# Kernel optimization log

Hardware: AMD Instinct MI355X
Metric: run time of the kernel (lower is better)

Reference implementation:

```python
import jax, jax.numpy as jnp
import numpy as np

RESO = 192
BASIS_DIM = 9
DATA_DIM = BASIS_DIM * 3 + 1  # 28 = sigma + 9 SH coeffs x 3 color channels
N_PTS = 1_000_000
RADIUS = 1.0


def setup_inputs() -> dict:
    key = jax.random.key(0)
    k1, k2, k3 = jax.random.split(key, 3)
    capacity = RESO ** 3
    # world-space points in [-1.1, 1.1] to exercise the border clamping
    points = jax.random.uniform(k1, (N_PTS, 3), jnp.float32, -1.1, 1.1)
    data = jax.random.normal(k2, (capacity, DATA_DIM), jnp.float32) * 0.1
    links = jnp.arange(capacity, dtype=jnp.int32)
    keep = jax.random.uniform(k3, (capacity,)) < 0.7
    links = jnp.where(keep, links, jnp.int32(-1)).reshape(RESO, RESO, RESO)
    radius = jnp.full((3,), RADIUS, jnp.float32)
    center = jnp.zeros((3,), jnp.float32)
    offset = 0.5 * (1.0 - center / radius)   # SparseGrid._offset
    scaling = 0.5 / radius                   # SparseGrid._scaling
    return {"points": points, "data": data, "links": links,
            "offset": offset, "scaling": scaling}


def _trilerp(points, data, links, offset, scaling):
    # world2grid: p = points * (scaling*gsz) + (offset*gsz - 0.5)
    gsz = jnp.array(links.shape, dtype=points.dtype)  # [3]
    p = points * (scaling * gsz) + (offset * gsz - 0.5)
    # clamp_min 0, clamp_max gsz[i]-1 (border padding)
    p = jnp.clip(p, 0.0, gsz - 1.0)
    # integer cell (trunc == floor since p >= 0), clamped to gsz[i]-2
    l = jnp.minimum(p.astype(jnp.int32), jnp.array(links.shape, jnp.int32) - 2)
    wb = p - l.astype(p.dtype)  # [N,3] fractional weights
    wa = 1.0 - wb
    lx, ly, lz = l[:, 0], l[:, 1], l[:, 2]

    def fetch(ix, iy, iz):
        lk = links[ix, iy, iz]                       # [N] int32, -1 = empty
        vals = data[jnp.maximum(lk, 0)]              # [N, C] gather
        return jnp.where((lk >= 0)[:, None], vals, jnp.zeros_like(vals))

    c000 = fetch(lx, ly, lz)
    c001 = fetch(lx, ly, lz + 1)
    c010 = fetch(lx, ly + 1, lz)
    c011 = fetch(lx, ly + 1, lz + 1)
    c100 = fetch(lx + 1, ly, lz)
    c101 = fetch(lx + 1, ly, lz + 1)
    c110 = fetch(lx + 1, ly + 1, lz)
    c111 = fetch(lx + 1, ly + 1, lz + 1)

    wz_a, wz_b = wa[:, 2:3], wb[:, 2:3]
    c00 = c000 * wz_a + c001 * wz_b
    c01 = c010 * wz_a + c011 * wz_b
    c10 = c100 * wz_a + c101 * wz_b
    c11 = c110 * wz_a + c111 * wz_b
    wy_a, wy_b = wa[:, 1:2], wb[:, 1:2]
    c0 = c00 * wy_a + c01 * wy_b
    c1 = c10 * wy_a + c11 * wy_b
    return c0 * wa[:, 0:1] + c1 * wb[:, 0:1]  # [N, 28]


def reference(points, data, links, offset, scaling):
    return _trilerp(points, data, links, offset, scaling)
```

## Files before the change

### kernel.cpp

```cpp
#include <hip/hip_runtime.h>

#define RESO 192
#define DATA_DIM 28

typedef float f4 __attribute__((ext_vector_type(4)));

__global__ __launch_bounds__(256) void trilerp_kernel(
    const float* __restrict__ points,
    const float* __restrict__ data,
    const int*   __restrict__ links,
    const float* __restrict__ offset,
    const float* __restrict__ scaling,
    float*       __restrict__ out,
    int npts)
{
    const int gid   = blockIdx.x * blockDim.x + threadIdx.x;
    const int point = gid >> 3;
    const int sub   = threadIdx.x & 7;
    if (point >= npts) return;

    const float px = points[point * 3 + 0];
    const float py = points[point * 3 + 1];
    const float pz = points[point * 3 + 2];

    const float g = (float)RESO;

    float p0 = px * (scaling[0] * g) + (offset[0] * g - 0.5f);
    float p1 = py * (scaling[1] * g) + (offset[1] * g - 0.5f);
    float p2 = pz * (scaling[2] * g) + (offset[2] * g - 0.5f);

    p0 = fminf(fmaxf(p0, 0.0f), g - 1.0f);
    p1 = fminf(fmaxf(p1, 0.0f), g - 1.0f);
    p2 = fminf(fmaxf(p2, 0.0f), g - 1.0f);

    const int lx = min((int)p0, RESO - 2);
    const int ly = min((int)p1, RESO - 2);
    const int lz = min((int)p2, RESO - 2);

    const float wbx = p0 - (float)lx, wax = 1.0f - wbx;
    const float wby = p1 - (float)ly, way = 1.0f - wby;
    const float wbz = p2 - (float)lz, waz = 1.0f - wbz;

    const int base = (lx * RESO + ly) * RESO + lz;
    const int lk000 = links[base];
    const int lk001 = links[base + 1];
    const int lk010 = links[base + RESO];
    const int lk011 = links[base + RESO + 1];
    const int lk100 = links[base + RESO * RESO];
    const int lk101 = links[base + RESO * RESO + 1];
    const int lk110 = links[base + RESO * RESO + RESO];
    const int lk111 = links[base + RESO * RESO + RESO + 1];

    if (sub >= 7) return;

    const float w000 = wax * way * waz;
    const float w001 = wax * way * wbz;
    const float w010 = wax * wby * waz;
    const float w011 = wax * wby * wbz;
    const float w100 = wbx * way * waz;
    const float w101 = wbx * way * wbz;
    const float w110 = wbx * wby * waz;
    const float w111 = wbx * wby * wbz;

    const int ch = sub * 4;

    f4 acc = (f4)(0.0f);

    #define CORNER(LK, W)                                                     \
        if ((LK) >= 0) {                                                      \
            const f4 v = *reinterpret_cast<const f4*>(                        \
                data + (size_t)(LK) * DATA_DIM + ch);                         \
            acc += (W) * v;                                                   \
        }

    CORNER(lk000, w000)
    CORNER(lk001, w001)
    CORNER(lk010, w010)
    CORNER(lk011, w011)
    CORNER(lk100, w100)
    CORNER(lk101, w101)
    CORNER(lk110, w110)
    CORNER(lk111, w111)
    #undef CORNER

    __builtin_nontemporal_store(acc,
        reinterpret_cast<f4*>(out + (size_t)point * DATA_DIM + ch));
}

extern "C" void kernel_launch(void* const* d_in, const int* in_sizes, int n_in,
                              void* d_out, int out_size, void* d_ws, size_t ws_size,
                              hipStream_t stream) {
    const float* points  = (const float*)d_in[0];
    const float* data    = (const float*)d_in[1];
    const int*   links   = (const int*)d_in[2];
    const float* offset  = (const float*)d_in[3];
    const float* scaling = (const float*)d_in[4];
    float* out = (float*)d_out;

    const int npts = in_sizes[0] / 3;

    const int blocks = (npts + 31) / 32;
    trilerp_kernel<<<blocks, 256, 0, stream>>>(points, data, links, offset,
                                               scaling, out, npts);
}
```

Before: 226.0 us.

## Bucket-sort points by spatial block before trilinear gather for locality

Adds a counting sort of the points into 16^3-voxel spatial buckets (zero, count with atomics, single-block scan, scatter), then runs the gather kernel over the sorted points and writes each result back to its original index. The goal is to make neighbouring threads touch nearby links and data rows, improving cache hit rates on the random 8-corner gathers from the large data table. In exchange it adds four extra launches, atomic contention and an extra pass over the points. Output writes also become scattered rather than coalesced. It falls back to the direct kernel when the workspace is too small.

```diff
diff --git a/kernel.cpp b/kernel.cpp
--- a/kernel.cpp
+++ b/kernel.cpp
@@ -2,10 +2,160 @@
 
 #define RESO 192
 #define DATA_DIM 28
+#define BSHIFT 4
+#define NBS ((RESO + (1 << BSHIFT) - 1) >> BSHIFT)
+#define NBUCKETS (NBS * NBS * NBS)
 
 typedef float f4 __attribute__((ext_vector_type(4)));
 
-__global__ __launch_bounds__(256) void trilerp_kernel(
+__device__ __forceinline__ void cell_of(float px, float py, float pz,
+                                        const float* __restrict__ offset,
+                                        const float* __restrict__ scaling,
+                                        int& lx, int& ly, int& lz,
+                                        float& p0, float& p1, float& p2) {
+    const float g = (float)RESO;
+    p0 = px * (scaling[0] * g) + (offset[0] * g - 0.5f);
+    p1 = py * (scaling[1] * g) + (offset[1] * g - 0.5f);
+    p2 = pz * (scaling[2] * g) + (offset[2] * g - 0.5f);
+    p0 = fminf(fmaxf(p0, 0.0f), g - 1.0f);
+    p1 = fminf(fmaxf(p1, 0.0f), g - 1.0f);
+    p2 = fminf(fmaxf(p2, 0.0f), g - 1.0f);
+    lx = min((int)p0, RESO - 2);
+    ly = min((int)p1, RESO - 2);
+    lz = min((int)p2, RESO - 2);
+}
+
+__global__ void zero_kernel(int* __restrict__ counts) {
+    int i = blockIdx.x * blockDim.x + threadIdx.x;
+    if (i < NBUCKETS) counts[i] = 0;
+}
+
+__global__ __launch_bounds__(256) void count_kernel(
+    const float* __restrict__ pts, const float* __restrict__ offset,
+    const float* __restrict__ scaling, int* __restrict__ counts, int npts) {
+    int i = blockIdx.x * blockDim.x + threadIdx.x;
+    if (i >= npts) return;
+    int lx, ly, lz; float p0, p1, p2;
+    cell_of(pts[i * 3], pts[i * 3 + 1], pts[i * 3 + 2], offset, scaling,
+            lx, ly, lz, p0, p1, p2);
+    int key = ((lx >> BSHIFT) * NBS + (ly >> BSHIFT)) * NBS + (lz >> BSHIFT);
+    atomicAdd(counts + key, 1);
+}
+
+__global__ __launch_bounds__(256) void scan_kernel(int* __restrict__ counts) {
+    __shared__ int part[256];
+    const int T = 256;
+    const int C = (NBUCKETS + T - 1) / T;
+    int t = threadIdx.x;
+    int local[(NBUCKETS + 255) / 256];
+    int s = 0;
+    for (int j = 0; j < C; ++j) {
+        int idx = t * C + j;
+        int v = (idx < NBUCKETS) ? counts[idx] : 0;
+        local[j] = s;
+        s += v;
+    }
+    part[t] = s;
+    __syncthreads();
+    for (int off = 1; off < T; off <<= 1) {
+        int v = (t >= off) ? part[t - off] : 0;
+        __syncthreads();
+        part[t] += v;
+        __syncthreads();
+    }
+    int base = (t == 0) ? 0 : part[t - 1];
+    for (int j = 0; j < C; ++j) {
+        int idx = t * C + j;
+        if (idx < NBUCKETS) counts[idx] = base + local[j];
+    }
+}
+
+__global__ __launch_bounds__(256) void scatter_kernel(
+    const float* __restrict__ pts, const float* __restrict__ offset,
+    const float* __restrict__ scaling, int* __restrict__ offsets,
+    f4* __restrict__ sorted, int npts) {
+    int i = blockIdx.x * blockDim.x + threadIdx.x;
+    if (i >= npts) return;
+    float px = pts[i * 3], py = pts[i * 3 + 1], pz = pts[i * 3 + 2];
+    int lx, ly, lz; float p0, p1, p2;
+    cell_of(px, py, pz, offset, scaling, lx, ly, lz, p0, p1, p2);
+    int key = ((lx >> BSHIFT) * NBS + (ly >> BSHIFT)) * NBS + (lz >> BSHIFT);
+    int pos = atomicAdd(offsets + key, 1);
+    f4 v = {px, py, pz, __int_as_float(i)};
+    sorted[pos] = v;
+}
+
+__global__ __launch_bounds__(256) void gather_kernel(
+    const f4* __restrict__ sorted,
+    const float* __restrict__ data,
+    const int*   __restrict__ links,
+    const float* __restrict__ offset,
+    const float* __restrict__ scaling,
+    float*       __restrict__ out,
+    int npts)
+{
+    const int gid   = blockIdx.x * blockDim.x + threadIdx.x;
+    const int point = gid >> 3;
+    const int sub   = threadIdx.x & 7;
+    if (point >= npts) return;
+
+    const f4 s = sorted[point];
+    const int orig = __float_as_int(s.w);
+
+    int lx, ly, lz; float p0, p1, p2;
+    cell_of(s.x, s.y, s.z, offset, scaling, lx, ly, lz, p0, p1, p2);
+
+    const float wbx = p0 - (float)lx, wax = 1.0f - wbx;
+    const float wby = p1 - (float)ly, way = 1.0f - wby;
+    const float wbz = p2 - (float)lz, waz = 1.0f - wbz;
+
+    const int base = (lx * RESO + ly) * RESO + lz;
+    const int lk000 = links[base];
+    const int lk001 = links[base + 1];
+    const int lk010 = links[base + RESO];
+    const int lk011 = links[base + RESO + 1];
+    const int lk100 = links[base + RESO * RESO];
+    const int lk101 = links[base + RESO * RESO + 1];
+    const int lk110 = links[base + RESO * RESO + RESO];
+    const int lk111 = links[base + RESO * RESO + RESO + 1];
+
+    if (sub >= 7) return;
+
+    const float w000 = wax * way * waz;
+    const float w001 = wax * way * wbz;
+    const float w010 = wax * wby * waz;
+    const float w011 = wax * wby * wbz;
+    const float w100 = wbx * way * waz;
+    const float w101 = wbx * way * wbz;
+    const float w110 = wbx * wby * waz;
+    const float w111 = wbx * wby * wbz;
+
+    const int ch = sub * 4;
+
+    f4 acc = {0.f, 0.f, 0.f, 0.f};
+
+    #define CORNER(LK, W)                                                     \
+        if ((LK) >= 0) {                                                      \
+            const f4 v = *reinterpret_cast<const f4*>(                        \
+                data + (size_t)(LK) * DATA_DIM + ch);                         \
+            acc += (W) * v;                                                   \
+        }
+
+    CORNER(lk000, w000)
+    CORNER(lk001, w001)
+    CORNER(lk010, w010)
+    CORNER(lk011, w011)
+    CORNER(lk100, w100)
+    CORNER(lk101, w101)
+    CORNER(lk110, w110)
+    CORNER(lk111, w111)
+    #undef CORNER
+
+    __builtin_nontemporal_store(acc,
+        reinterpret_cast<f4*>(out + (size_t)orig * DATA_DIM + ch));
+}
+
+__global__ __launch_bounds__(256) void trilerp_direct(
     const float* __restrict__ points,
     const float* __restrict__ data,
     const int*   __restrict__ links,
@@ -19,23 +169,9 @@
     const int sub   = threadIdx.x & 7;
     if (point >= npts) return;
 
-    const float px = points[point * 3 + 0];
-    const float py = points[point * 3 + 1];
-    const float pz = points[point * 3 + 2];
-
-    const float g = (float)RESO;
-
-    float p0 = px * (scaling[0] * g) + (offset[0] * g - 0.5f);
-    float p1 = py * (scaling[1] * g) + (offset[1] * g - 0.5f);
-    float p2 = pz * (scaling[2] * g) + (offset[2] * g - 0.5f);
-
-    p0 = fminf(fmaxf(p0, 0.0f), g - 1.0f);
-    p1 = fminf(fmaxf(p1, 0.0f), g - 1.0f);
-    p2 = fminf(fmaxf(p2, 0.0f), g - 1.0f);
-
-    const int lx = min((int)p0, RESO - 2);
-    const int ly = min((int)p1, RESO - 2);
-    const int lz = min((int)p2, RESO - 2);
+    int lx, ly, lz; float p0, p1, p2;
+    cell_of(points[point * 3], points[point * 3 + 1], points[point * 3 + 2],
+            offset, scaling, lx, ly, lz, p0, p1, p2);
 
     const float wbx = p0 - (float)lx, wax = 1.0f - wbx;
     const float wby = p1 - (float)ly, way = 1.0f - wby;
@@ -63,8 +199,7 @@
     const float w111 = wbx * wby * wbz;
 
     const int ch = sub * 4;
-
-    f4 acc = (f4)(0.0f);
+    f4 acc = {0.f, 0.f, 0.f, 0.f};
 
     #define CORNER(LK, W)                                                     \
         if ((LK) >= 0) {                                                      \
@@ -72,7 +207,6 @@
                 data + (size_t)(LK) * DATA_DIM + ch);                         \
             acc += (W) * v;                                                   \
         }
-
     CORNER(lk000, w000)
     CORNER(lk001, w001)
     CORNER(lk010, w010)
@@ -99,7 +233,26 @@
 
     const int npts = in_sizes[0] / 3;
 
-    const int blocks = (npts + 31) / 32;
-    trilerp_kernel<<<blocks, 256, 0, stream>>>(points, data, links, offset,
+    const size_t need = (size_t)NBUCKETS * sizeof(int) + (size_t)npts * sizeof(f4);
+    if (ws_size < need) {
+        const int blocks = (npts + 31) / 32;
+        trilerp_direct<<<blocks, 256, 0, stream>>>(points, data, links, offset,
+                                                   scaling, out, npts);
+        return;
+    }
+
+    int* counts = (int*)d_ws;
+    f4*  sorted = (f4*)((char*)d_ws + (size_t)NBUCKETS * sizeof(int));
+
+    const int pblocks = (npts + 255) / 256;
+
+    zero_kernel<<<(NBUCKETS + 255) / 256, 256, 0, stream>>>(counts);
+    count_kernel<<<pblocks, 256, 0, stream>>>(points, offset, scaling, counts, npts);
+    scan_kernel<<<1, 256, 0, stream>>>(counts);
+    scatter_kernel<<<pblocks, 256, 0, stream>>>(points, offset, scaling, counts,
+                                                sorted, npts);
+
+    const int gblocks = (npts + 31) / 32;
+    gather_kernel<<<gblocks, 256, 0, stream>>>(sorted, data, links, offset,
                                                scaling, out, npts);
 }
```

Measured after the change: 584.6 us. 159% more time.
